# Kernel tuning notes

Hardware: AMD Instinct MI355X
Metric: run time of the kernel (lower is better)

The kernel has to match this reference:

```python
import jax, jax.numpy as jnp
import numpy as np

B, N1, N2 = 4, 1024, 4096
CIN, C, DM, K = 512, 256, 256, 16
BN_EPS = 1e-5  # eval-mode BatchNorm1d with init running stats (mean=0, var=1)

def square_distance(a, b):
    # ||a_i - b_j||^2 via -2ab + a^2 + b^2 (matches torch square_distance)
    return (jnp.sum(a * a, -1)[:, :, None] + jnp.sum(b * b, -1)[:, None, :]
            - 2.0 * jnp.einsum('bnd,bmd->bnm', a, b))

def index_points(pts, idx):
    # pts: [B,N,C], idx: [B,M,K] -> [B,M,K,C]
    return jax.vmap(lambda p, i: p[i])(pts, idx)

def setup_inputs():
    key = jax.random.key(0)
    ks = jax.random.split(key, 20)
    rnd = lambda i, shape: jax.random.normal(ks[i], shape, jnp.float32) * 0.05
    return dict(
        xyz1=jax.random.normal(ks[0], (B, N1, 3), jnp.float32),
        points1=jax.random.normal(ks[1], (B, N1, CIN), jnp.float32),
        xyz2=jax.random.normal(ks[2], (B, N2, 3), jnp.float32),
        points2=jax.random.normal(ks[3], (B, N2, C), jnp.float32),
        up_w1=rnd(4, (CIN, C)), up_b1=jnp.zeros((C,), jnp.float32),
        up_w2=rnd(5, (C, C)), up_b2=jnp.zeros((C,), jnp.float32),
        fc1_w=rnd(6, (C, DM)), fc1_b=jnp.zeros((DM,), jnp.float32),
        fc2_w=rnd(7, (DM, C)), fc2_b=jnp.zeros((C,), jnp.float32),
        delta_w1=rnd(8, (3, DM)), delta_b1=jnp.zeros((DM,), jnp.float32),
        delta_w2=rnd(9, (DM, DM)), delta_b2=jnp.zeros((DM,), jnp.float32),
        gamma_w1=rnd(10, (DM, DM)), gamma_b1=jnp.zeros((DM,), jnp.float32),
        gamma_w2=rnd(11, (DM, DM)), gamma_b2=jnp.zeros((DM,), jnp.float32),
        wq=rnd(12, (DM, DM)), wk=rnd(13, (DM, DM)), wv=rnd(14, (DM, DM)),
    )

def reference(xyz1, points1, xyz2, points2, up_w1, up_b1, up_w2, up_b2,
              fc1_w, fc1_b, fc2_w, fc2_b, delta_w1, delta_b1, delta_w2, delta_b2,
              gamma_w1, gamma_b1, gamma_w2, gamma_b2, wq, wk, wv):
    bn = 1.0 / jnp.sqrt(1.0 + BN_EPS)
    # --- TransitionUp ---
    f1 = jax.nn.relu((points1 @ up_w1 + up_b1) * bn)   # [B,N1,C]
    f2 = jax.nn.relu((points2 @ up_w2 + up_b2) * bn)   # [B,N2,C]
    d = square_distance(xyz2, xyz1)                    # [B,N2,N1]
    negd, idx3 = jax.lax.top_k(-d, 3)                  # 3 nearest coarse points
    recip = 1.0 / (-negd + 1e-8)
    w = recip / jnp.sum(recip, -1, keepdims=True)      # [B,N2,3]
    interp = jnp.sum(index_points(f1, idx3) * w[..., None], axis=2)
    feats = interp + f2                                # [B,N2,C]
    # --- TransformerBlock (Point-Transformer vector attention) ---
    dd = square_distance(xyz2, xyz2)                   # [B,N2,N2]
    _, knn = jax.lax.top_k(-dd, K)                     # [B,N2,K]
    knn_xyz = index_points(xyz2, knn)                  # [B,N2,K,3]
    x = feats @ fc1_w + fc1_b                          # [B,N2,DM]
    q = x @ wq
    kf = index_points(x @ wk, knn)                     # [B,N2,K,DM]
    vf = index_points(x @ wv, knn)
    rel = xyz2[:, :, None, :] - knn_xyz
    pos = jax.nn.relu(rel @ delta_w1 + delta_b1) @ delta_w2 + delta_b2
    a = q[:, :, None, :] - kf + pos
    a = jax.nn.relu(a @ gamma_w1 + gamma_b1) @ gamma_w2 + gamma_b2
    a = jax.nn.softmax(a / jnp.sqrt(jnp.float32(DM)), axis=-2)  # softmax over K
    res = jnp.sum(a * (vf + pos), axis=2)              # [B,N2,DM]
    out = res @ fc2_w + fc2_b + feats                  # residual
    return (xyz2, out)
```

## Files before the change

### kernel.cpp

```cpp
#include <hip/hip_runtime.h>
#include <hip/hip_bf16.h>
#include <math.h>
#include <float.h>

#define BB   4
#define N1   1024
#define N2   4096
#define CIN  512
#define CC   256
#define DM   256
#define KNNK 16
#define PPB  2

typedef __attribute__((ext_vector_type(8))) short bf16x8;
typedef __attribute__((ext_vector_type(4))) float f32x4;

__device__ __forceinline__ float bf16r(float x) {
    return __bfloat162float(__float2bfloat16(x));
}
__device__ __forceinline__ unsigned short f2bu(float x) {
    __hip_bfloat16 h = __float2bfloat16(x);
    return *reinterpret_cast<unsigned short*>(&h);
}
__device__ __forceinline__ float bu2f(unsigned short u) {
    __hip_bfloat16 h = *reinterpret_cast<__hip_bfloat16*>(&u);
    return __bfloat162float(h);
}

struct SwzArgs {
    const float* W[10];
    unsigned short* B[10];
    int K[10];
};
__global__ __launch_bounds__(256) void swizzle_all(SwzArgs a)
{
    int m = blockIdx.y;
    int idx = blockIdx.x * 256 + threadIdx.x;
    int total = (a.K[m] >> 5) << 10;
    if (idx >= total) return;
    const float* W = a.W[m];
    unsigned short* B = a.B[m];
    int l = idx & 63;
    int tile = (idx >> 6) & 15;
    int kb = idx >> 10;
    int col = tile * 16 + (l & 15);
    int k0 = kb * 32 + ((l >> 4) << 3);
#pragma unroll
    for (int i = 0; i < 8; ++i)
        B[(size_t)idx * 8 + i] = f2bu(W[(size_t)(k0 + i) * 256 + col]);
}

template<int KD, int NT, bool RELU, bool BN_, bool RESID>
__global__ __launch_bounds__(256) void gemm_mfma(
    const float* __restrict__ X, const unsigned short* __restrict__ Bw,
    const float* __restrict__ bias, const float* __restrict__ resid,
    float scale, float* __restrict__ Y)
{
    const int NSPLIT = 16 / NT;
    const int c = threadIdx.x;
    const int l = c & 63, wv_ = c >> 6;
    const int lr = l & 15, lg = l >> 4;
    const int row0 = (blockIdx.x / NSPLIT) * 64;
    const int tb = (blockIdx.x % NSPLIT) * NT;
    __shared__ __align__(16) unsigned short As[64][72];

    f32x4 acc[NT];
#pragma unroll
    for (int t = 0; t < NT; ++t) acc[t] = (f32x4){0.f, 0.f, 0.f, 0.f};

    const int rs = c >> 2, c0 = (c & 3) * 16;
    for (int ks = 0; ks < KD / 64; ++ks) {
        const float* src = X + (size_t)(row0 + rs) * KD + ks * 64 + c0;
#pragma unroll
        for (int i = 0; i < 16; i += 4) {
            float4 v = *(const float4*)(src + i);
            As[rs][c0 + i + 0] = f2bu(v.x);
            As[rs][c0 + i + 1] = f2bu(v.y);
            As[rs][c0 + i + 2] = f2bu(v.z);
            As[rs][c0 + i + 3] = f2bu(v.w);
        }
        __syncthreads();
#pragma unroll
        for (int kbl = 0; kbl < 2; ++kbl) {
            int kb = ks * 2 + kbl;
            bf16x8 af = *(const bf16x8*)&As[wv_ * 16 + lr][kbl * 32 + lg * 8];
#pragma unroll
            for (int t = 0; t < NT; ++t) {
                bf16x8 bf = *(const bf16x8*)&Bw[((size_t)(kb * 16 + tb + t) * 64 + l) * 8];
                acc[t] = __builtin_amdgcn_mfma_f32_16x16x32_bf16(af, bf, acc[t], 0, 0, 0);
            }
        }
        __syncthreads();
    }
#pragma unroll
    for (int t = 0; t < NT; ++t) {
        int col = (tb + t) * 16 + lr;
        float bb = bias ? bias[col] : 0.f;
#pragma unroll
        for (int r = 0; r < 4; ++r) {
            size_t row = row0 + wv_ * 16 + lg * 4 + r;
            float v = bf16r(acc[t][r]);
            v = bf16r(v + bb);
            if (BN_) v = bf16r(v * scale);
            if (RELU) v = fmaxf(v, 0.f);
            if (RESID) v = bf16r(v + resid[row * 256 + col]);
            Y[row * 256 + col] = v;
        }
    }
}

__global__ __launch_bounds__(256) void qkv_mfma(
    const float* __restrict__ X,
    const unsigned short* __restrict__ Bq,
    const unsigned short* __restrict__ Bk,
    const unsigned short* __restrict__ Bv,
    float* __restrict__ Yq, float* __restrict__ Yk, float* __restrict__ Yv)
{
    const int NT = 8;
    const int c = threadIdx.x;
    const int l = c & 63, wv_ = c >> 6;
    const int lr = l & 15, lg = l >> 4;
    const int row0 = (blockIdx.x >> 1) * 64;
    const int tb = (blockIdx.x & 1) * NT;
    __shared__ __align__(16) unsigned short As[64][72];

    f32x4 aq[NT], ak[NT], av_[NT];
#pragma unroll
    for (int t = 0; t < NT; ++t) {
        aq[t] = (f32x4){0.f, 0.f, 0.f, 0.f};
        ak[t] = aq[t]; av_[t] = aq[t];
    }

    const int rs = c >> 2, c0 = (c & 3) * 16;
    for (int ks = 0; ks < CC / 64; ++ks) {
        const float* src = X + (size_t)(row0 + rs) * CC + ks * 64 + c0;
#pragma unroll
        for (int i = 0; i < 16; i += 4) {
            float4 v = *(const float4*)(src + i);
            As[rs][c0 + i + 0] = f2bu(v.x);
            As[rs][c0 + i + 1] = f2bu(v.y);
            As[rs][c0 + i + 2] = f2bu(v.z);
            As[rs][c0 + i + 3] = f2bu(v.w);
        }
        __syncthreads();
#pragma unroll
        for (int kbl = 0; kbl < 2; ++kbl) {
            int kb = ks * 2 + kbl;
            bf16x8 af = *(const bf16x8*)&As[wv_ * 16 + lr][kbl * 32 + lg * 8];
#pragma unroll
            for (int t = 0; t < NT; ++t) {
                size_t fo = ((size_t)(kb * 16 + tb + t) * 64 + l) * 8;
                bf16x8 bq = *(const bf16x8*)&Bq[fo];
                bf16x8 bk = *(const bf16x8*)&Bk[fo];
                bf16x8 bv = *(const bf16x8*)&Bv[fo];
                aq[t]  = __builtin_amdgcn_mfma_f32_16x16x32_bf16(af, bq, aq[t], 0, 0, 0);
                ak[t]  = __builtin_amdgcn_mfma_f32_16x16x32_bf16(af, bk, ak[t], 0, 0, 0);
                av_[t] = __builtin_amdgcn_mfma_f32_16x16x32_bf16(af, bv, av_[t], 0, 0, 0);
            }
        }
        __syncthreads();
    }
#pragma unroll
    for (int t = 0; t < NT; ++t) {
        int col = (tb + t) * 16 + lr;
#pragma unroll
        for (int r = 0; r < 4; ++r) {
            size_t row = row0 + wv_ * 16 + lg * 4 + r;
            Yq[row * 256 + col] = bf16r(aq[t][r]);
            Yk[row * 256 + col] = bf16r(ak[t][r]);
            Yv[row * 256 + col] = bf16r(av_[t][r]);
        }
    }
}

__device__ __forceinline__ float norm2_ref(float x, float y, float z) {
    return __fadd_rn(__fadd_rn(__fmul_rn(x, x), __fmul_rn(y, y)), __fmul_rn(z, z));
}
__device__ __forceinline__ float dist_ref(float sa, float nb,
                                          float ax, float ay, float az,
                                          float bx, float by, float bz) {
    float dot = __fadd_rn(__fadd_rn(__fmul_rn(ax, bx), __fmul_rn(ay, by)),
                          __fmul_rn(az, bz));
    return __fsub_rn(__fadd_rn(sa, nb), __fmul_rn(2.f, dot));
}

__global__ __launch_bounds__(256) void nn3_interp_kernel(
    const float* __restrict__ xyz1, const float* __restrict__ xyz2,
    const float* __restrict__ f1, float* __restrict__ feats)
{
    const int b = blockIdx.x >> 6;
    const int q0 = (blockIdx.x & 63) << 6;
    const int tid = threadIdx.x;
    const int ql = tid >> 2, r = tid & 3;
    const int n = q0 + ql;
    __shared__ float sx[N1], sy[N1], sz[N1], snb[N1];
    __shared__ float sd[64][4][3];
    __shared__ int   si[64][4][3];
    __shared__ float sw[64][3];
    __shared__ int   sidx[64][3];
    for (int i = tid; i < N1; i += 256) {
        const float* p = xyz1 + ((size_t)b * N1 + i) * 3;
        float x = p[0], y = p[1], z = p[2];
        sx[i] = x; sy[i] = y; sz[i] = z;
        snb[i] = norm2_ref(x, y, z);
    }
    __syncthreads();
    const float* pq = xyz2 + ((size_t)b * N2 + n) * 3;
    const float ax = pq[0], ay = pq[1], az = pq[2];
    const float sa = norm2_ref(ax, ay, az);
    float d0 = FLT_MAX, d1 = FLT_MAX, d2 = FLT_MAX;
    int i0 = 0, i1 = 0, i2 = 0;
    const int jb = r << 8;
    for (int jj = 0; jj < 256; ++jj) {
        int j = jb + jj;
        float dist = dist_ref(sa, snb[j], ax, ay, az, sx[j], sy[j], sz[j]);
        if (dist < d2) {
            if (dist < d1) {
                d2 = d1; i2 = i1;
                if (dist < d0) { d1 = d0; i1 = i0; d0 = dist; i0 = j; }
                else           { d1 = dist; i1 = j; }
            } else { d2 = dist; i2 = j; }
        }
    }
    sd[ql][r][0] = d0; sd[ql][r][1] = d1; sd[ql][r][2] = d2;
    si[ql][r][0] = i0; si[ql][r][1] = i1; si[ql][r][2] = i2;
    __syncthreads();
    if (r == 0) {
        int p0 = 0, p1 = 0, p2 = 0, p3 = 0;
        float md[3]; int mi[3];
        for (int o = 0; o < 3; ++o) {
            float h0 = (p0 < 3) ? sd[ql][0][p0] : FLT_MAX;
            float h1 = (p1 < 3) ? sd[ql][1][p1] : FLT_MAX;
            float h2 = (p2 < 3) ? sd[ql][2][p2] : FLT_MAX;
            float h3 = (p3 < 3) ? sd[ql][3][p3] : FLT_MAX;
            int br = 0; float bd = h0;
            if (h1 < bd) { bd = h1; br = 1; }
            if (h2 < bd) { bd = h2; br = 2; }
            if (h3 < bd) { bd = h3; br = 3; }
            if (br == 0)      { mi[o] = si[ql][0][p0]; md[o] = h0; ++p0; }
            else if (br == 1) { mi[o] = si[ql][1][p1]; md[o] = h1; ++p1; }
            else if (br == 2) { mi[o] = si[ql][2][p2]; md[o] = h2; ++p2; }
            else              { mi[o] = si[ql][3][p3]; md[o] = h3; ++p3; }
        }
        float r0 = __fdiv_rn(1.f, __fadd_rn(md[0], 1e-8f));
        float r1 = __fdiv_rn(1.f, __fadd_rn(md[1], 1e-8f));
        float r2 = __fdiv_rn(1.f, __fadd_rn(md[2], 1e-8f));
        float s  = __fadd_rn(__fadd_rn(r0, r1), r2);
        sw[ql][0] = __fdiv_rn(r0, s);
        sw[ql][1] = __fdiv_rn(r1, s);
        sw[ql][2] = __fdiv_rn(r2, s);
        sidx[ql][0] = mi[0]; sidx[ql][1] = mi[1]; sidx[ql][2] = mi[2];
    }
    __syncthreads();
    const float* f1b = f1 + (size_t)b * N1 * 256;
    for (int p = 0; p < 64; ++p) {
        int bn = (b << 12) + q0 + p;
        float w0 = sw[p][0], w1 = sw[p][1], w2 = sw[p][2];
        int j0 = sidx[p][0], j1 = sidx[p][1], j2 = sidx[p][2];
        float itp = w0 * f1b[(size_t)j0 * 256 + tid]
                  + w1 * f1b[(size_t)j1 * 256 + tid]
                  + w2 * f1b[(size_t)j2 * 256 + tid];
        feats[(size_t)bn * 256 + tid] = bf16r(bf16r(itp) + feats[(size_t)bn * 256 + tid]);
    }
}

__global__ __launch_bounds__(256) void knn_kernel(
    const float* __restrict__ xyz2, int* __restrict__ knn_out)
{
    const int b = blockIdx.x >> 6;
    const int q0 = (blockIdx.x & 63) << 6;
    const int tid = threadIdx.x;
    const int ql = tid >> 2, r = tid & 3;
    const int n = q0 + ql;
    __shared__ float sx[N2], sy[N2], sz[N2], sn[N2];
    __shared__ float sd[64][4][16];
    __shared__ int   si[64][4][16];
    for (int i = tid; i < N2; i += 256) {
        const float* p = xyz2 + ((size_t)b * N2 + i) * 3;
        float x = p[0], y = p[1], z = p[2];
        sx[i] = x; sy[i] = y; sz[i] = z;
        sn[i] = norm2_ref(x, y, z);
    }
    __syncthreads();
    const float ax = sx[n], ay = sy[n], az = sz[n];
    const float sa = sn[n];
    float d[16]; int id[16];
#pragma unroll
    for (int s = 0; s < 16; ++s) { d[s] = FLT_MAX; id[s] = 0; }
    const int jbase = r << 10;
    for (int jj = 0; jj < 1024; ++jj) {
        int j = jbase + jj;
        float dist = dist_ref(sa, sn[j], ax, ay, az, sx[j], sy[j], sz[j]);
        if (dist < d[15]) {
#pragma unroll
            for (int s = 15; s >= 0; --s) {
                bool shift = (s > 0) && (dist < d[s - 1]);
                bool place = (dist < d[s]) && !shift;
                float nd = shift ? d[s - 1] : (place ? dist : d[s]);
                int   ni = shift ? id[s - 1] : (place ? j : id[s]);
                d[s] = nd; id[s] = ni;
            }
        }
    }
#pragma unroll
    for (int s = 0; s < 16; ++s) { sd[ql][r][s] = d[s]; si[ql][r][s] = id[s]; }
    __syncthreads();
    if (r == 0) {
        int p0 = 0, p1 = 0, p2 = 0, p3 = 0;
        size_t ob = ((size_t)b * N2 + n) * 16;
        for (int o = 0; o < 16; ++o) {
            float h0 = (p0 < 16) ? sd[ql][0][p0] : FLT_MAX;
            float h1 = (p1 < 16) ? sd[ql][1][p1] : FLT_MAX;
            float h2 = (p2 < 16) ? sd[ql][2][p2] : FLT_MAX;
            float h3 = (p3 < 16) ? sd[ql][3][p3] : FLT_MAX;
            int br = 0; float bd = h0;
            if (h1 < bd) { bd = h1; br = 1; }
            if (h2 < bd) { bd = h2; br = 2; }
            if (h3 < bd) { bd = h3; br = 3; }
            int bi;
            if (br == 0)      { bi = si[ql][0][p0]; ++p0; }
            else if (br == 1) { bi = si[ql][1][p1]; ++p1; }
            else if (br == 2) { bi = si[ql][2][p2]; ++p2; }
            else              { bi = si[ql][3][p3]; ++p3; }
            knn_out[ob + o] = bi;
        }
    }
}

__global__ __launch_bounds__(256) void attn_mfma2(
    const float* __restrict__ xyz2, const float* __restrict__ qg,
    const float* __restrict__ kg, const float* __restrict__ vg,
    const int* __restrict__ knn,
    const float* __restrict__ d1w, const float* __restrict__ d1b,
    const float* __restrict__ d2b, const float* __restrict__ g1b,
    const float* __restrict__ g2b,
    const unsigned short* __restrict__ Bd2,
    const unsigned short* __restrict__ Bg1,
    const unsigned short* __restrict__ Bg2,
    float* __restrict__ res)
{
    const int bn0 = blockIdx.x * PPB;
    const int b = bn0 >> 12;
    const int c = threadIdx.x;
    const int l = c & 63, wv_ = c >> 6;
    const int lr = l & 15, lg = l >> 4;

    __shared__ __align__(16) unsigned short phb[PPB * 16][264];
    __shared__ __align__(16) unsigned short posb[PPB * 16][264];
    __shared__ int   knn_s[PPB][16];
    __shared__ float relx[PPB][16], rely[PPB][16], relz[PPB][16];

    if (c < PPB * 16) {
        int p = c >> 4, kk = c & 15;
        int idx = knn[(size_t)(bn0 + p) * 16 + kk];
        knn_s[p][kk] = idx;
        const float* pq = xyz2 + (size_t)(bn0 + p) * 3;
        const float* pk = xyz2 + ((size_t)b * N2 + idx) * 3;
        relx[p][kk] = bf16r(pq[0] - pk[0]);
        rely[p][kk] = bf16r(pq[1] - pk[1]);
        relz[p][kk] = bf16r(pq[2] - pk[2]);
    }
    __syncthreads();

    const size_t basebc = (size_t)b * N2 * 256;
    float kf[PPB][16], qv[PPB];
#pragma unroll
    for (int p = 0; p < PPB; ++p) {
        qv[p] = qg[(size_t)(bn0 + p) * 256 + c];
#pragma unroll
        for (int kk = 0; kk < 16; ++kk)
            kf[p][kk] = kg[basebc + (size_t)knn_s[p][kk] * 256 + c];
    }

    {
        float w0 = bf16r(d1w[c]), w1 = bf16r(d1w[256 + c]), w2 = bf16r(d1w[512 + c]);
        float bb = d1b[c];
#pragma unroll
        for (int p = 0; p < PPB; ++p)
#pragma unroll
            for (int kk = 0; kk < 16; ++kk) {
                float v = fmaf(relx[p][kk], w0, fmaf(rely[p][kk], w1, fmaf(relz[p][kk], w2, bb)));
                phb[p * 16 + kk][c] = f2bu(fmaxf(v, 0.f));
            }
    }
    __syncthreads();

    f32x4 acc[PPB][4];
#pragma unroll
    for (int p = 0; p < PPB; ++p)
#pragma unroll
        for (int t = 0; t < 4; ++t) acc[p][t] = (f32x4){0.f, 0.f, 0.f, 0.f};
    for (int kb = 0; kb < 8; ++kb) {
        bf16x8 bfr[4];
#pragma unroll
        for (int t = 0; t < 4; ++t)
            bfr[t] = *(const bf16x8*)&Bd2[((size_t)(kb * 16 + wv_ * 4 + t) * 64 + l) * 8];
#pragma unroll
        for (int p = 0; p < PPB; ++p) {
            bf16x8 af = *(const bf16x8*)&phb[p * 16 + lr][kb * 32 + lg * 8];
#pragma unroll
            for (int t = 0; t < 4; ++t)
                acc[p][t] = __builtin_amdgcn_mfma_f32_16x16x32_bf16(af, bfr[t], acc[p][t], 0, 0, 0);
        }
    }
#pragma unroll
    for (int p = 0; p < PPB; ++p)
#pragma unroll
        for (int t = 0; t < 4; ++t) {
            int col = (wv_ * 4 + t) * 16 + lr;
            float bb = d2b[col];
#pragma unroll
            for (int r = 0; r < 4; ++r)
                posb[p * 16 + lg * 4 + r][col] = f2bu(acc[p][t][r] + bb);
        }
    __syncthreads();

    float posr[PPB][16];
#pragma unroll
    for (int p = 0; p < PPB; ++p)
#pragma unroll
        for (int kk = 0; kk < 16; ++kk) posr[p][kk] = bu2f(posb[p * 16 + kk][c]);
#pragma unroll
    for (int p = 0; p < PPB; ++p)
#pragma unroll
        for (int kk = 0; kk < 16; ++kk)
            phb[p * 16 + kk][c] = f2bu(bf16r(qv[p] - kf[p][kk]) + posr[p][kk]);
    __syncthreads();

#pragma unroll
    for (int p = 0; p < PPB; ++p)
#pragma unroll
        for (int t = 0; t < 4; ++t) acc[p][t] = (f32x4){0.f, 0.f, 0.f, 0.f};
    for (int kb = 0; kb < 8; ++kb) {
        bf16x8 bfr[4];
#pragma unroll
        for (int t = 0; t < 4; ++t)
            bfr[t] = *(const bf16x8*)&Bg1[((size_t)(kb * 16 + wv_ * 4 + t) * 64 + l) * 8];
#pragma unroll
        for (int p = 0; p < PPB; ++p) {
            bf16x8 af = *(const bf16x8*)&phb[p * 16 + lr][kb * 32 + lg * 8];
#pragma unroll
            for (int t = 0; t < 4; ++t)
                acc[p][t] = __builtin_amdgcn_mfma_f32_16x16x32_bf16(af, bfr[t], acc[p][t], 0, 0, 0);
        }
    }
    __syncthreads();
#pragma unroll
    for (int p = 0; p < PPB; ++p)
#pragma unroll
        for (int t = 0; t < 4; ++t) {
            int col = (wv_ * 4 + t) * 16 + lr;
            float bb = g1b[col];
#pragma unroll
            for (int r = 0; r < 4; ++r)
                phb[p * 16 + lg * 4 + r][col] = f2bu(fmaxf(acc[p][t][r] + bb, 0.f));
        }
    __syncthreads();

#pragma unroll
    for (int p = 0; p < PPB; ++p)
#pragma unroll
        for (int t = 0; t < 4; ++t) acc[p][t] = (f32x4){0.f, 0.f, 0.f, 0.f};
    for (int kb = 0; kb < 8; ++kb) {
        bf16x8 bfr[4];
#pragma unroll
        for (int t = 0; t < 4; ++t)
            bfr[t] = *(const bf16x8*)&Bg2[((size_t)(kb * 16 + wv_ * 4 + t) * 64 + l) * 8];
#pragma unroll
        for (int p = 0; p < PPB; ++p) {
            bf16x8 af = *(const bf16x8*)&phb[p * 16 + lr][kb * 32 + lg * 8];
#pragma unroll
            for (int t = 0; t < 4; ++t)
                acc[p][t] = __builtin_amdgcn_mfma_f32_16x16x32_bf16(af, bfr[t], acc[p][t], 0, 0, 0);
        }
    }
#pragma unroll
    for (int p = 0; p < PPB; ++p)
#pragma unroll
        for (int t = 0; t < 4; ++t) {
            int col = (wv_ * 4 + t) * 16 + lr;
            float bb = g2b[col];
#pragma unroll
            for (int r = 0; r < 4; ++r)
                posb[p * 16 + lg * 4 + r][col] = f2bu(acc[p][t][r] + bb);
        }
    __syncthreads();

#pragma unroll
    for (int p = 0; p < PPB; ++p) {
        float av[16];
#pragma unroll
        for (int kk = 0; kk < 16; ++kk) av[kk] = bu2f(posb[p * 16 + kk][c]) * 0.0625f;
        float m = av[0];
#pragma unroll
        for (int kk = 1; kk < 16; ++kk) m = fmaxf(m, av[kk]);
        float e[16];
        float s = 0.f;
#pragma unroll
        for (int kk = 0; kk < 16; ++kk) {
            e[kk] = bf16r(expf(av[kk] - m));
            s += e[kk];
        }
#pragma unroll
        for (int kk = 0; kk < 16; ++kk) e[kk] = bf16r(e[kk] / s);
        float rr = 0.f;
#pragma unroll
        for (int kk = 0; kk < 16; ++kk) {
            float vfv = vg[basebc + (size_t)knn_s[p][kk] * 256 + c];
            float vp = bf16r(vfv + posr[p][kk]);
            rr = fmaf(e[kk], vp, rr);
        }
        res[(size_t)(bn0 + p) * 256 + c] = bf16r(rr);
    }
}

extern "C" void kernel_launch(void* const* d_in, const int* in_sizes, int n_in,
                              void* d_out, int out_size, void* d_ws, size_t ws_size,
                              hipStream_t stream)
{
    const float* xyz1     = (const float*)d_in[0];
    const float* points1  = (const float*)d_in[1];
    const float* xyz2     = (const float*)d_in[2];
    const float* points2  = (const float*)d_in[3];
    const float* up_w1    = (const float*)d_in[4];
    const float* up_b1    = (const float*)d_in[5];
    const float* up_w2    = (const float*)d_in[6];
    const float* up_b2    = (const float*)d_in[7];
    const float* fc1_w    = (const float*)d_in[8];
    const float* fc1_b    = (const float*)d_in[9];
    const float* fc2_w    = (const float*)d_in[10];
    const float* fc2_b    = (const float*)d_in[11];
    const float* delta_w1 = (const float*)d_in[12];
    const float* delta_b1 = (const float*)d_in[13];
    const float* delta_w2 = (const float*)d_in[14];
    const float* delta_b2 = (const float*)d_in[15];
    const float* gamma_w1 = (const float*)d_in[16];
    const float* gamma_b1 = (const float*)d_in[17];
    const float* gamma_w2 = (const float*)d_in[18];
    const float* gamma_b2 = (const float*)d_in[19];
    const float* wq       = (const float*)d_in[20];
    const float* wk       = (const float*)d_in[21];
    const float* wv       = (const float*)d_in[22];

    float* ws = (float*)d_ws;
    float* f1    = ws;
    float* feats = f1 + (size_t)BB * N1 * 256;
    float* x     = feats + (size_t)BB * N2 * 256;
    float* qb    = x + (size_t)BB * N2 * 256;
    float* kb    = qb + (size_t)BB * N2 * 256;
    float* vb    = kb + (size_t)BB * N2 * 256;
    int*   knn   = (int*)(vb + (size_t)BB * N2 * 256);
    unsigned short* Bd2  = (unsigned short*)(knn + (size_t)BB * N2 * 16);
    unsigned short* Bg1  = Bd2 + 65536;
    unsigned short* Bg2  = Bg1 + 65536;
    unsigned short* Bup1 = Bg2 + 65536;
    unsigned short* Bup2 = Bup1 + 131072;
    unsigned short* Bfc1 = Bup2 + 65536;
    unsigned short* Bfc2 = Bfc1 + 65536;
    unsigned short* Bq   = Bfc2 + 65536;
    unsigned short* Bk   = Bq + 65536;
    unsigned short* Bv   = Bk + 65536;
    float* resb = x;

    float* out = (float*)d_out;
    hipMemcpyAsync(out, xyz2, (size_t)BB * N2 * 3 * sizeof(float),
                   hipMemcpyDeviceToDevice, stream);

    const float BN = (float)(1.0 / sqrt(1.0 + 1e-5));

    SwzArgs sa;
    sa.W[0] = up_w1;    sa.B[0] = Bup1; sa.K[0] = CIN;
    sa.W[1] = up_w2;    sa.B[1] = Bup2; sa.K[1] = CC;
    sa.W[2] = fc1_w;    sa.B[2] = Bfc1; sa.K[2] = CC;
    sa.W[3] = fc2_w;    sa.B[3] = Bfc2; sa.K[3] = CC;
    sa.W[4] = wq;       sa.B[4] = Bq;   sa.K[4] = CC;
    sa.W[5] = wk;       sa.B[5] = Bk;   sa.K[5] = CC;
    sa.W[6] = wv;       sa.B[6] = Bv;   sa.K[6] = CC;
    sa.W[7] = delta_w2; sa.B[7] = Bd2;  sa.K[7] = CC;
    sa.W[8] = gamma_w1; sa.B[8] = Bg1;  sa.K[8] = CC;
    sa.W[9] = gamma_w2; sa.B[9] = Bg2;  sa.K[9] = CC;
    swizzle_all<<<dim3(64, 10), 256, 0, stream>>>(sa);

    gemm_mfma<CC, 8, true, true, false><<<BB * N2 / 64 * 2, 256, 0, stream>>>(
        points2, Bup2, up_b2, nullptr, BN, feats);
    gemm_mfma<CIN, 4, true, true, false><<<BB * N1 / 64 * 4, 256, 0, stream>>>(
        points1, Bup1, up_b1, nullptr, BN, f1);
    nn3_interp_kernel<<<BB * 64, 256, 0, stream>>>(xyz1, xyz2, f1, feats);
    gemm_mfma<CC, 8, false, false, false><<<BB * N2 / 64 * 2, 256, 0, stream>>>(
        feats, Bfc1, fc1_b, nullptr, 1.f, x);
    qkv_mfma<<<BB * N2 / 64 * 2, 256, 0, stream>>>(x, Bq, Bk, Bv, qb, kb, vb);
    knn_kernel<<<BB * 64, 256, 0, stream>>>(xyz2, knn);
    attn_mfma2<<<BB * N2 / PPB, 256, 0, stream>>>(xyz2, qb, kb, vb, knn,
                                                  delta_w1, delta_b1, delta_b2, gamma_b1, gamma_b2,
                                                  Bd2, Bg1, Bg2, resb);
    gemm_mfma<CC, 8, false, false, true><<<BB * N2 / 64 * 2, 256, 0, stream>>>(
        resb, Bfc2, fc2_b, feats, 1.f, out + (size_t)BB * N2 * 3);
}
```

Measured before the change: 637.4 us.

## Split kNN search across 16 threads per query with packed float4 points

Adds a pack kernel that precomputes xyz plus squared norm into a float4 buffer. The kNN kernel now uses 16 threads per query, each scanning 256 candidates, with 4x more blocks (1024 instead of 256), and the shared-memory staging of all points is dropped in favour of L1/L2-cached global float4 loads. The goal is more occupancy and parallelism across the CUs for the serial top-16 insertion. In exchange, the final merge is 16-way and runs on one thread per query, and every thread loads candidates from global memory.

```diff
diff --git a/kernel.cpp b/kernel.cpp
--- a/kernel.cpp
+++ b/kernel.cpp
@@ -182,6 +182,16 @@
     float dot = __fadd_rn(__fadd_rn(__fmul_rn(ax, bx), __fmul_rn(ay, by)),
                           __fmul_rn(az, bz));
     return __fsub_rn(__fadd_rn(sa, nb), __fmul_rn(2.f, dot));
+}
+
+__global__ __launch_bounds__(256) void pack_kernel(
+    const float* __restrict__ xyz2, float4* __restrict__ pk)
+{
+    int i = blockIdx.x * 256 + threadIdx.x;
+    if (i >= BB * N2) return;
+    const float* p = xyz2 + (size_t)i * 3;
+    float x = p[0], y = p[1], z = p[2];
+    pk[i] = make_float4(x, y, z, norm2_ref(x, y, z));
 }
 
 __global__ __launch_bounds__(256) void nn3_interp_kernel(
@@ -265,32 +275,28 @@
 }
 
 __global__ __launch_bounds__(256) void knn_kernel(
-    const float* __restrict__ xyz2, int* __restrict__ knn_out)
-{
-    const int b = blockIdx.x >> 6;
-    const int q0 = (blockIdx.x & 63) << 6;
+    const float4* __restrict__ pk, int* __restrict__ knn_out)
+{
+    const int b = blockIdx.x >> 8;
+    const int q0 = (blockIdx.x & 255) << 4;
     const int tid = threadIdx.x;
-    const int ql = tid >> 2, r = tid & 3;
+    const int ql = tid >> 4, t = tid & 15;
     const int n = q0 + ql;
-    __shared__ float sx[N2], sy[N2], sz[N2], sn[N2];
-    __shared__ float sd[64][4][16];
-    __shared__ int   si[64][4][16];
-    for (int i = tid; i < N2; i += 256) {
-        const float* p = xyz2 + ((size_t)b * N2 + i) * 3;
-        float x = p[0], y = p[1], z = p[2];
-        sx[i] = x; sy[i] = y; sz[i] = z;
-        sn[i] = norm2_ref(x, y, z);
-    }
-    __syncthreads();
-    const float ax = sx[n], ay = sy[n], az = sz[n];
-    const float sa = sn[n];
+    __shared__ float sd[16][16][16];
+    __shared__ int   si[16][16][16];
+
+    const float4* base = pk + (size_t)b * N2;
+    float4 qp = base[n];
+    const float ax = qp.x, ay = qp.y, az = qp.z, sa = qp.w;
+
     float d[16]; int id[16];
 #pragma unroll
     for (int s = 0; s < 16; ++s) { d[s] = FLT_MAX; id[s] = 0; }
-    const int jbase = r << 10;
-    for (int jj = 0; jj < 1024; ++jj) {
+    const int jbase = t << 8;
+    for (int jj = 0; jj < 256; ++jj) {
         int j = jbase + jj;
-        float dist = dist_ref(sa, sn[j], ax, ay, az, sx[j], sy[j], sz[j]);
+        float4 cp = base[j];
+        float dist = dist_ref(sa, cp.w, ax, ay, az, cp.x, cp.y, cp.z);
         if (dist < d[15]) {
 #pragma unroll
             for (int s = 15; s >= 0; --s) {
@@ -303,26 +309,22 @@
         }
     }
 #pragma unroll
-    for (int s = 0; s < 16; ++s) { sd[ql][r][s] = d[s]; si[ql][r][s] = id[s]; }
-    __syncthreads();
-    if (r == 0) {
-        int p0 = 0, p1 = 0, p2 = 0, p3 = 0;
+    for (int s = 0; s < 16; ++s) { sd[ql][t][s] = d[s]; si[ql][t][s] = id[s]; }
+    __syncthreads();
+    if (t == 0) {
+        int ptr[16];
+#pragma unroll
+        for (int u = 0; u < 16; ++u) ptr[u] = 0;
         size_t ob = ((size_t)b * N2 + n) * 16;
         for (int o = 0; o < 16; ++o) {
-            float h0 = (p0 < 16) ? sd[ql][0][p0] : FLT_MAX;
-            float h1 = (p1 < 16) ? sd[ql][1][p1] : FLT_MAX;
-            float h2 = (p2 < 16) ? sd[ql][2][p2] : FLT_MAX;
-            float h3 = (p3 < 16) ? sd[ql][3][p3] : FLT_MAX;
-            int br = 0; float bd = h0;
-            if (h1 < bd) { bd = h1; br = 1; }
-            if (h2 < bd) { bd = h2; br = 2; }
-            if (h3 < bd) { bd = h3; br = 3; }
-            int bi;
-            if (br == 0)      { bi = si[ql][0][p0]; ++p0; }
-            else if (br == 1) { bi = si[ql][1][p1]; ++p1; }
-            else if (br == 2) { bi = si[ql][2][p2]; ++p2; }
-            else              { bi = si[ql][3][p3]; ++p3; }
-            knn_out[ob + o] = bi;
+            int bu = 0;
+            float bd = (ptr[0] < 16) ? sd[ql][0][ptr[0]] : FLT_MAX;
+            for (int u = 1; u < 16; ++u) {
+                float hu = (ptr[u] < 16) ? sd[ql][u][ptr[u]] : FLT_MAX;
+                if (hu < bd) { bd = hu; bu = u; }
+            }
+            knn_out[ob + o] = si[ql][bu][ptr[bu]];
+            ++ptr[bu];
         }
     }
 }
@@ -560,6 +562,7 @@
     unsigned short* Bq   = Bfc2 + 65536;
     unsigned short* Bk   = Bq + 65536;
     unsigned short* Bv   = Bk + 65536;
+    float4* pkbuf = (float4*)(Bv + 65536);
     float* resb = x;
 
     float* out = (float*)d_out;
@@ -581,6 +584,8 @@
     sa.W[9] = gamma_w2; sa.B[9] = Bg2;  sa.K[9] = CC;
     swizzle_all<<<dim3(64, 10), 256, 0, stream>>>(sa);
 
+    pack_kernel<<<BB * N2 / 256, 256, 0, stream>>>(xyz2, pkbuf);
+
     gemm_mfma<CC, 8, true, true, false><<<BB * N2 / 64 * 2, 256, 0, stream>>>(
         points2, Bup2, up_b2, nullptr, BN, feats);
     gemm_mfma<CIN, 4, true, true, false><<<BB * N1 / 64 * 4, 256, 0, stream>>>(
@@ -589,7 +594,7 @@
     gemm_mfma<CC, 8, false, false, false><<<BB * N2 / 64 * 2, 256, 0, stream>>>(
         feats, Bfc1, fc1_b, nullptr, 1.f, x);
     qkv_mfma<<<BB * N2 / 64 * 2, 256, 0, stream>>>(x, Bq, Bk, Bv, qb, kb, vb);
-    knn_kernel<<<BB * 64, 256, 0, stream>>>(xyz2, knn);
+    knn_kernel<<<BB * 256, 256, 0, stream>>>(pkbuf, knn);
     attn_mfma2<<<BB * N2 / PPB, 256, 0, stream>>>(xyz2, qb, kb, vb, knn,
                                                   delta_w1, delta_b1, delta_b2, gamma_b1, gamma_b2,
                                                   Bd2, Bg1, Bg2, resb);
```

Measured after the change: 631.3 us. Within noise of the previous version (-1.0%).
